# Performance work log

Measured on AMD Instinct MI355X. Metric: run time of the kernel, lower is better.

Reference implementation:

```python
import jax, jax.numpy as jnp
import numpy as np

ALPHA = 0.0005625
N_SLOPE = 1.5
VT = 0.026
VD = 0.1
BN_EPS = 1e-5


def _log1p_exp(a):
    return jnp.log1p(jnp.exp(jnp.clip(a, -30.0, 30.0)))


def _ekv_conv(x, theta, stride=1, padding=1):
    # x: (B, C, H, W); theta: (Cout, C*3*3)
    # Patches ordered (C, kh, kw) along channel dim, matching torch.nn.Unfold.
    patches = jax.lax.conv_general_dilated_patches(
        x, filter_shape=(3, 3), window_strides=(stride, stride),
        padding=[(padding, padding), (padding, padding)])
    B, K, Ho, Wo = patches.shape
    vg = patches.reshape(B, 1, K, Ho * Wo)              # (B,1,K,L)
    th = theta[None, :, :, None]                        # (1,Cout,K,1)
    nVT = N_SLOPE * VT
    arg1 = (vg - th) / nVT
    arg2 = (vg - th - VD) / nVT
    I = ALPHA * (_log1p_exp(arg1) ** 2 - _log1p_exp(arg2) ** 2)  # (B,Cout,K,L)
    return I.sum(axis=2).reshape(B, -1, Ho, Wo)


def _batchnorm_train(x, gamma, beta):
    # training-mode BN (biased variance), matching fresh nn.BatchNorm2d forward
    mean = x.mean(axis=(0, 2, 3), keepdims=True)
    var = x.var(axis=(0, 2, 3), keepdims=True)
    xhat = (x - mean) * jax.lax.rsqrt(var + BN_EPS)
    return xhat * gamma[None, :, None, None] + beta[None, :, None, None]


def setup_inputs() -> dict:
    key = jax.random.key(0)
    ks = jax.random.split(key, 3)
    B, C, H, W = 4, 64, 32, 32
    planes = 64
    K = C * 9
    x = jax.random.uniform(ks[0], (B, C, H, W), dtype=jnp.float32)
    theta1 = jax.random.uniform(ks[1], (planes, K), minval=2.8, maxval=4.8, dtype=jnp.float32)
    theta2 = jax.random.uniform(ks[2], (planes, planes * 9), minval=2.8, maxval=4.8, dtype=jnp.float32)
    return {
        "x": x,
        "theta1": theta1,
        "theta2": theta2,
        "prescale_scale": jnp.float32(4.5),
        "prescale_shift": jnp.float32(3.8),
        "ls1": jnp.float32(3.0),
        "ls2": jnp.float32(3.0),
        "bn1_gamma": jnp.ones((planes,), jnp.float32),
        "bn1_beta": jnp.zeros((planes,), jnp.float32),
        "bn2_gamma": jnp.ones((planes,), jnp.float32),
        "bn2_beta": jnp.zeros((planes,), jnp.float32),
    }


def reference(x, theta1, theta2, prescale_scale, prescale_shift, ls1, ls2,
              bn1_gamma, bn1_beta, bn2_gamma, bn2_beta):
    identity = x  # stride==1 and in_planes==planes -> identity shortcut
    out = x * prescale_scale + prescale_shift
    out = ls1 * _ekv_conv(out, theta1, stride=1, padding=1)
    out = _batchnorm_train(out, bn1_gamma, bn1_beta)
    out = ls2 * _ekv_conv(out, theta2, stride=1, padding=1)
    out = _batchnorm_train(out, bn2_gamma, bn2_beta)
    return out + identity
```

## Files before the change

kernel.cpp:

```cpp
#include <hip/hip_runtime.h>
#include <math.h>

#define NLUT     4096
#define LUT_LO   (-0.33)
#define LUT_H    (0.0004)
#define LUT_INVH (2500.0f)
#define LUT_BIAS (825.0f)
#define BAND_LO  (-0.35f)
#define BAND_HI  (1.28f)

#define WS_LUT    0
#define WS_TH2T   32768
#define WS_RAW1   180224
#define WS_MASK   1228800
#define WS_STAT1  1261568
#define WS_SUMS2  1262080
#define WS_THMAX  1262592
#define WS_THMIN  1262596
#define WS_TOTAL  1262600

__device__ __forceinline__ double f_exact(double d) {
    const double nvt = 1.5 * 0.026;
    double a1 = d / nvt;         a1 = fmin(fmax(a1, -30.0), 30.0);
    double a2 = (d - 0.1) / nvt; a2 = fmin(fmax(a2, -30.0), 30.0);
    double s1 = log1p(exp(a1));
    double s2 = log1p(exp(a2));
    return 0.0005625 * (s1 * s1 - s2 * s2);
}

__global__ __launch_bounds__(256) void k0_prep(const float* __restrict__ theta2,
        float* __restrict__ lutg, float* __restrict__ th2t, unsigned* __restrict__ mm)
{
    int blk = blockIdx.x;
    if (blk < 16) {
        int i = blk * 256 + threadIdx.x;
        double f0 = f_exact(LUT_LO + (double)i * LUT_H);
        double f1 = f_exact(LUT_LO + (double)(i + 1) * LUT_H);
        lutg[2 * i]     = (float)f0;
        lutg[2 * i + 1] = (float)(f1 - f0);
    } else {
        int i = (blk - 16) * 256 + threadIdx.x;
        int p = i & 63, k = i >> 6;
        float v = theta2[p * 576 + k];
        th2t[k * 64 + p] = v;
        __shared__ float smin[256], smax[256];
        smin[threadIdx.x] = v; smax[threadIdx.x] = v;
        __syncthreads();
        for (int s = 128; s > 0; s >>= 1) {
            if (threadIdx.x < s) {
                smin[threadIdx.x] = fminf(smin[threadIdx.x], smin[threadIdx.x + s]);
                smax[threadIdx.x] = fmaxf(smax[threadIdx.x], smax[threadIdx.x + s]);
            }
            __syncthreads();
        }
        if (threadIdx.x == 0) {
            atomicMax(&mm[0], __float_as_uint(smax[0]));
            atomicMin(&mm[1], __float_as_uint(smin[0]));
        }
    }
}

__global__ __launch_bounds__(256) void k1_conv1(const float* __restrict__ x,
    const float* __restrict__ theta1, const float* __restrict__ psc,
    const float* __restrict__ psh, const float* __restrict__ ls1,
    const float* __restrict__ lutg, float* __restrict__ raw1)
{
    __shared__ float2 lut[NLUT];
    {
        const float4* src = (const float4*)lutg;
        float4* dst = (float4*)lut;
        #pragma unroll
        for (int i = threadIdx.x; i < NLUT / 2; i += 256) dst[i] = src[i];
    }
    __syncthreads();

    int blk = blockIdx.x;
    int pg = blk & 7;
    int yp = (blk >> 3) & 15;
    int b  = blk >> 7;
    int wv = __builtin_amdgcn_readfirstlane((int)threadIdx.x >> 6);
    int lane = threadIdx.x & 63;
    int r = lane >> 5, xc = lane & 31;
    int y = yp * 2 + r;
    int p0 = pg * 8 + wv * 2;

    float scale = psc[0], shift = psh[0];
    const float* xb  = x + b * 65536;
    const float* t0p = theta1 + p0 * 576;
    const float* t1p = t0p + 576;
    float acc0 = 0.f, acc1 = 0.f;

    #pragma unroll
    for (int j = 0; j < 9; ++j) {
        int ny = y + j / 3 - 1, nx = xc + j % 3 - 1;
        if ((unsigned)ny < 32u && (unsigned)nx < 32u) {
            const float* px = xb + ny * 32 + nx;
            #pragma unroll 4
            for (int c = 0; c < 64; ++c) {
                float v  = fmaf(px[c * 1024], scale, shift);
                float t0 = t0p[c * 9 + j];
                float t1 = t1p[c * 9 + j];
                float q0 = fmaf(v - t0, LUT_INVH, LUT_BIAS);
                q0 = fminf(fmaxf(q0, 0.f), 4095.0f);
                int   i0 = (int)q0;
                float fr0 = q0 - (float)i0;
                float2 e0 = lut[i0];
                acc0 = fmaf(fr0, e0.y, acc0 + e0.x);
                float q1 = fmaf(v - t1, LUT_INVH, LUT_BIAS);
                q1 = fminf(fmaxf(q1, 0.f), 4095.0f);
                int   i1 = (int)q1;
                float fr1 = q1 - (float)i1;
                float2 e1 = lut[i1];
                acc1 = fmaf(fr1, e1.y, acc1 + e1.x);
            }
        }
    }
    float l1 = ls1[0];
    int o = ((b * 64 + p0) * 32 + y) * 32 + xc;
    raw1[o]        = l1 * acc0;
    raw1[o + 1024] = l1 * acc1;
}

__global__ __launch_bounds__(256) void k2_stats1(const float* __restrict__ raw1,
                                                 float* __restrict__ stat1)
{
    int p = blockIdx.x;
    float s = 0.f, q = 0.f;
    for (int b = 0; b < 4; ++b) {
        const float* base = raw1 + (b * 64 + p) * 1024;
        for (int k = threadIdx.x; k < 1024; k += 256) {
            float v = base[k];
            s += v; q += v * v;
        }
    }
    __shared__ float ss[256], sq[256];
    ss[threadIdx.x] = s; sq[threadIdx.x] = q;
    __syncthreads();
    for (int st = 128; st > 0; st >>= 1) {
        if (threadIdx.x < st) {
            ss[threadIdx.x] += ss[threadIdx.x + st];
            sq[threadIdx.x] += sq[threadIdx.x + st];
        }
        __syncthreads();
    }
    if (threadIdx.x == 0) {
        double mean = (double)ss[0] / 4096.0;
        double var  = (double)sq[0] / 4096.0 - mean * mean;
        if (var < 0) var = 0;
        stat1[p]      = (float)mean;
        stat1[64 + p] = (float)(1.0 / sqrt(var + 1e-5));
    }
}

__global__ __launch_bounds__(256) void k3_bn1mask(float* __restrict__ v2,
    const float* __restrict__ stat1, const float* __restrict__ g1,
    const float* __restrict__ b1, const unsigned* __restrict__ mm,
    unsigned long long* __restrict__ masks)
{
    int idx = blockIdx.x * 256 + threadIdx.x;
    int c = (idx >> 10) & 63;
    float v = v2[idx];
    v = (v - stat1[c]) * stat1[64 + c];
    v = v * g1[c] + b1[c];
    v2[idx] = v;
    float tmax = __uint_as_float(mm[0]);
    float tmin = __uint_as_float(mm[1]);
    if (v > tmin + BAND_LO && v < tmax + BAND_HI) {
        int b = idx >> 16;
        int pix = idx & 1023;
        atomicOr(&masks[b * 1024 + pix], 1ull << c);
    }
}

__global__ __launch_bounds__(256) void k4_conv2(const float* __restrict__ v2,
    const float* __restrict__ th2t, const unsigned long long* __restrict__ masks,
    const float* __restrict__ ls2, float* __restrict__ out, float* __restrict__ sums2)
{
    int wv = __builtin_amdgcn_readfirstlane((int)threadIdx.x >> 6);
    int lane = threadIdx.x & 63;
    int W = blockIdx.x * 4 + wv;
    float l2 = ls2[0];
    const float inv_nvt = (float)(1.0 / (1.5 * 0.026));
    float lsum = 0.f, lsq = 0.f;

    for (int i = 0; i < 4; ++i) {
        int P = W * 4 + i;
        int b = P >> 10, rem = P & 1023;
        int y = rem >> 5, xq = rem & 31;
        float acc = 0.f;
        #pragma unroll
        for (int j = 0; j < 9; ++j) {
            int ny = y + j / 3 - 1, nx = xq + j % 3 - 1;
            if ((unsigned)ny < 32u && (unsigned)nx < 32u) {
                unsigned long long m = masks[b * 1024 + ny * 32 + nx];
                while (m) {
                    int c = __ffsll((long long)m) - 1;
                    m &= m - 1;
                    float v  = v2[((b * 64 + c) * 32 + ny) * 32 + nx];
                    float th = th2t[(c * 9 + j) * 64 + lane];
                    float d = v - th;
                    if (d > BAND_LO && d < BAND_HI) {
                        float a1 = fminf(fmaxf(d * inv_nvt, -30.f), 30.f);
                        float a2 = fminf(fmaxf((d - 0.1f) * inv_nvt, -30.f), 30.f);
                        float s1 = __logf(1.f + __expf(a1));
                        float s2 = __logf(1.f + __expf(a2));
                        acc += (s1 * s1 - s2 * s2);
                    }
                }
            }
        }
        float r2 = 0.0005625f * l2 * acc;
        out[((b * 64 + lane) * 32 + y) * 32 + xq] = r2;
        lsum += r2; lsq += r2 * r2;
    }
    __shared__ float ss[256], sq[256];
    ss[threadIdx.x] = lsum; sq[threadIdx.x] = lsq;
    __syncthreads();
    if (threadIdx.x < 64) {
        float a  = ss[threadIdx.x] + ss[threadIdx.x + 64] + ss[threadIdx.x + 128] + ss[threadIdx.x + 192];
        float qq = sq[threadIdx.x] + sq[threadIdx.x + 64] + sq[threadIdx.x + 128] + sq[threadIdx.x + 192];
        atomicAdd(&sums2[threadIdx.x], a);
        atomicAdd(&sums2[64 + threadIdx.x], qq);
    }
}

__global__ __launch_bounds__(256) void k6_final(float* __restrict__ out,
    const float* __restrict__ x, const float* __restrict__ sums2,
    const float* __restrict__ g2, const float* __restrict__ b2)
{
    int idx = blockIdx.x * 256 + threadIdx.x;
    int p = (idx >> 10) & 63;
    float m   = sums2[p] * (1.f / 4096.f);
    float var = sums2[64 + p] * (1.f / 4096.f) - m * m;
    var = fmaxf(var, 0.f);
    float rstd = rsqrtf(var + 1e-5f);
    out[idx] = (out[idx] - m) * rstd * g2[p] + b2[p] + x[idx];
}

extern "C" void kernel_launch(void* const* d_in, const int* in_sizes, int n_in,
                              void* d_out, int out_size, void* d_ws, size_t ws_size,
                              hipStream_t stream)
{
    const float* x   = (const float*)d_in[0];
    const float* th1 = (const float*)d_in[1];
    const float* th2 = (const float*)d_in[2];
    const float* psc = (const float*)d_in[3];
    const float* psh = (const float*)d_in[4];
    const float* l1  = (const float*)d_in[5];
    const float* l2  = (const float*)d_in[6];
    const float* g1  = (const float*)d_in[7];
    const float* b1  = (const float*)d_in[8];
    const float* g2  = (const float*)d_in[9];
    const float* b2  = (const float*)d_in[10];
    float* out = (float*)d_out;
    char* ws = (char*)d_ws;
    if (ws_size < (size_t)WS_TOTAL) return;

    float* lut   = (float*)(ws + WS_LUT);
    float* th2t  = (float*)(ws + WS_TH2T);
    float* raw1  = (float*)(ws + WS_RAW1);
    unsigned long long* masks = (unsigned long long*)(ws + WS_MASK);
    float* stat1 = (float*)(ws + WS_STAT1);
    float* sums2 = (float*)(ws + WS_SUMS2);
    unsigned* mm = (unsigned*)(ws + WS_THMAX);

    hipMemsetAsync(ws + WS_MASK, 0, WS_THMIN - WS_MASK, stream);
    hipMemsetAsync(ws + WS_THMIN, 0x7F, 4, stream);

    k0_prep  <<<160,  256, 0, stream>>>(th2, lut, th2t, mm);
    k1_conv1 <<<512,  256, 0, stream>>>(x, th1, psc, psh, l1, lut, raw1);
    k2_stats1<<<64,   256, 0, stream>>>(raw1, stat1);
    k3_bn1mask<<<1024,256, 0, stream>>>(raw1, stat1, g1, b1, mm, masks);
    k4_conv2 <<<256,  256, 0, stream>>>(raw1, th2t, masks, l2, out, sums2);
    k6_final <<<1024, 256, 0, stream>>>(out, x, sums2, g2, b2);
}
```

Measured before the change: 95.27 us.

## Shrink LUT, pre-transform input to NHWC, fuse BN1 stats into conv1

The LUT drops from 4096 to 1024 entries with a folded slope/intercept encoding, so each tap needs one fmaf plus a masked byte-offset lookup. The prescale is precomputed into a channel-last buffer (aliasing the output) so conv1 reads float4 vectors of channels. BN1 statistics are now accumulated with wave shuffles and atomics inside conv1, which removes the separate stats kernel and one launch. Conv2 goes from four pixels per wave to one, with four times as many blocks, and the min/max init is folded into a single memset using complemented atomicMax. In exchange the coarser LUT can lose accuracy, and float atomics make the BN1 sums order-nondeterministic.

```diff
diff --git a/kernel.cpp b/kernel.cpp
--- a/kernel.cpp
+++ b/kernel.cpp
@@ -1,23 +1,22 @@
 #include <hip/hip_runtime.h>
 #include <math.h>
 
-#define NLUT     4096
-#define LUT_LO   (-0.33)
-#define LUT_H    (0.0004)
-#define LUT_INVH (2500.0f)
-#define LUT_BIAS (825.0f)
-#define BAND_LO  (-0.35f)
-#define BAND_HI  (1.28f)
+#define LUT_N   1024
+#define LUT_H   0.0016
+#define LUT_LO  (-0.33)
+#define INVH8   5000.0f
+#define QMAX    8184.0f
+#define BAND_LO (-0.35f)
+#define BAND_HI (1.28f)
 
 #define WS_LUT    0
-#define WS_TH2T   32768
-#define WS_RAW1   180224
-#define WS_MASK   1228800
-#define WS_STAT1  1261568
-#define WS_SUMS2  1262080
-#define WS_THMAX  1262592
-#define WS_THMIN  1262596
-#define WS_TOTAL  1262600
+#define WS_TH2T   8192
+#define WS_RAW1   155648
+#define WS_MASK   1204224
+#define WS_SUMS1  1236992
+#define WS_SUMS2  1237504
+#define WS_MM     1238016
+#define WS_TOTAL  1238024
 
 __device__ __forceinline__ double f_exact(double d) {
     const double nvt = 1.5 * 0.026;
@@ -28,146 +27,135 @@
     return 0.0005625 * (s1 * s1 - s2 * s2);
 }
 
-__global__ __launch_bounds__(256) void k0_prep(const float* __restrict__ theta2,
-        float* __restrict__ lutg, float* __restrict__ th2t, unsigned* __restrict__ mm)
-{
-    int blk = blockIdx.x;
-    if (blk < 16) {
-        int i = blk * 256 + threadIdx.x;
-        double f0 = f_exact(LUT_LO + (double)i * LUT_H);
-        double f1 = f_exact(LUT_LO + (double)(i + 1) * LUT_H);
-        lutg[2 * i]     = (float)f0;
-        lutg[2 * i + 1] = (float)(f1 - f0);
-    } else {
-        int i = (blk - 16) * 256 + threadIdx.x;
+__global__ __launch_bounds__(256) void k0_prep(
+    const float* __restrict__ x, const float* __restrict__ theta2,
+    const float* __restrict__ psc, const float* __restrict__ psh,
+    float2* __restrict__ lutg, float* __restrict__ th2t,
+    float* __restrict__ xs, unsigned* __restrict__ mm)
+{
+    int blk = blockIdx.x, tid = threadIdx.x;
+    if (blk < 4) {
+        int i = blk * 256 + tid;
+        double d0 = LUT_LO + (double)i * LUT_H;
+        double f0 = f_exact(d0), f1 = f_exact(d0 + LUT_H);
+        double d8 = (f1 - f0) * 0.125;
+        double ex = f0 - (double)(8 * i) * d8;
+        lutg[i] = make_float2((float)ex, (float)d8);
+    } else if (blk < 148) {
+        int i = (blk - 4) * 256 + tid;
         int p = i & 63, k = i >> 6;
         float v = theta2[p * 576 + k];
         th2t[k * 64 + p] = v;
         __shared__ float smin[256], smax[256];
-        smin[threadIdx.x] = v; smax[threadIdx.x] = v;
+        smin[tid] = v; smax[tid] = v;
         __syncthreads();
         for (int s = 128; s > 0; s >>= 1) {
-            if (threadIdx.x < s) {
-                smin[threadIdx.x] = fminf(smin[threadIdx.x], smin[threadIdx.x + s]);
-                smax[threadIdx.x] = fmaxf(smax[threadIdx.x], smax[threadIdx.x + s]);
+            if (tid < s) {
+                smin[tid] = fminf(smin[tid], smin[tid + s]);
+                smax[tid] = fmaxf(smax[tid], smax[tid + s]);
             }
             __syncthreads();
         }
-        if (threadIdx.x == 0) {
+        if (tid == 0) {
             atomicMax(&mm[0], __float_as_uint(smax[0]));
-            atomicMin(&mm[1], __float_as_uint(smin[0]));
-        }
-    }
-}
-
-__global__ __launch_bounds__(256) void k1_conv1(const float* __restrict__ x,
-    const float* __restrict__ theta1, const float* __restrict__ psc,
-    const float* __restrict__ psh, const float* __restrict__ ls1,
-    const float* __restrict__ lutg, float* __restrict__ raw1)
-{
-    __shared__ float2 lut[NLUT];
+            atomicMax(&mm[1], ~__float_as_uint(smin[0]));
+        }
+    } else {
+        int idx = (blk - 148) * 256 + tid;
+        int c = idx & 63, gp = idx >> 6;
+        int b = gp >> 10, pp = gp & 1023;
+        float xv = x[b * 65536 + c * 1024 + pp];
+        float sc = psc[0] * INVH8;
+        float sh = (psh[0] + 0.33f) * INVH8;
+        xs[idx] = fmaf(xv, sc, sh);
+    }
+}
+
+#define TAP(V, TH) {                                            \
+    float th_ = (TH);                                           \
+    float q_ = fmaf(th_, -INVH8, (V));                          \
+    q_ = fminf(fmaxf(q_, 0.f), QMAX);                           \
+    int ib_ = (int)q_ & ~7;                                     \
+    float2 e_ = *(const float2*)((const char*)lut + ib_);       \
+    acc = fmaf(q_, e_.y, acc + e_.x);                           \
+}
+
+__global__ __launch_bounds__(256) void k1_conv1(
+    const float* __restrict__ xs, const float* __restrict__ theta1,
+    const float* __restrict__ ls1, const float2* __restrict__ lutg,
+    float* __restrict__ raw1, float* __restrict__ sums1)
+{
+    __shared__ float2 lut[LUT_N];
     {
-        const float4* src = (const float4*)lutg;
-        float4* dst = (float4*)lut;
-        #pragma unroll
-        for (int i = threadIdx.x; i < NLUT / 2; i += 256) dst[i] = src[i];
+        const float4* s = (const float4*)lutg;
+        float4* d = (float4*)lut;
+        for (int i = threadIdx.x; i < LUT_N / 2; i += 256) d[i] = s[i];
     }
     __syncthreads();
 
     int blk = blockIdx.x;
-    int pg = blk & 7;
-    int yp = (blk >> 3) & 15;
-    int b  = blk >> 7;
     int wv = __builtin_amdgcn_readfirstlane((int)threadIdx.x >> 6);
     int lane = threadIdx.x & 63;
+    int p  = (blk & 15) * 4 + wv;
+    int yp = (blk >> 4) & 15;
+    int b  = blk >> 8;
     int r = lane >> 5, xc = lane & 31;
     int y = yp * 2 + r;
-    int p0 = pg * 8 + wv * 2;
-
-    float scale = psc[0], shift = psh[0];
-    const float* xb  = x + b * 65536;
-    const float* t0p = theta1 + p0 * 576;
-    const float* t1p = t0p + 576;
-    float acc0 = 0.f, acc1 = 0.f;
-
-    #pragma unroll
-    for (int j = 0; j < 9; ++j) {
-        int ny = y + j / 3 - 1, nx = xc + j % 3 - 1;
-        if ((unsigned)ny < 32u && (unsigned)nx < 32u) {
-            const float* px = xb + ny * 32 + nx;
+
+    const float* tpp = theta1 + p * 576;
+    float acc = 0.f;
+
+    for (int jy = 0; jy < 3; ++jy) {
+        int ny = y + jy - 1;
+        if ((unsigned)ny >= 32u) continue;
+        for (int jx = 0; jx < 3; ++jx) {
+            int nx = xc + jx - 1;
+            if ((unsigned)nx >= 32u) continue;
+            const float4* px4 = (const float4*)(xs + (((b << 10) + ny * 32 + nx) << 6));
+            const float* tp = tpp + (jy * 3 + jx);
             #pragma unroll 4
-            for (int c = 0; c < 64; ++c) {
-                float v  = fmaf(px[c * 1024], scale, shift);
-                float t0 = t0p[c * 9 + j];
-                float t1 = t1p[c * 9 + j];
-                float q0 = fmaf(v - t0, LUT_INVH, LUT_BIAS);
-                q0 = fminf(fmaxf(q0, 0.f), 4095.0f);
-                int   i0 = (int)q0;
-                float fr0 = q0 - (float)i0;
-                float2 e0 = lut[i0];
-                acc0 = fmaf(fr0, e0.y, acc0 + e0.x);
-                float q1 = fmaf(v - t1, LUT_INVH, LUT_BIAS);
-                q1 = fminf(fmaxf(q1, 0.f), 4095.0f);
-                int   i1 = (int)q1;
-                float fr1 = q1 - (float)i1;
-                float2 e1 = lut[i1];
-                acc1 = fmaf(fr1, e1.y, acc1 + e1.x);
+            for (int cc = 0; cc < 16; ++cc) {
+                float4 vb = px4[cc];
+                const float* tq = tp + cc * 36;
+                TAP(vb.x, tq[0]);
+                TAP(vb.y, tq[9]);
+                TAP(vb.z, tq[18]);
+                TAP(vb.w, tq[27]);
             }
         }
     }
-    float l1 = ls1[0];
-    int o = ((b * 64 + p0) * 32 + y) * 32 + xc;
-    raw1[o]        = l1 * acc0;
-    raw1[o + 1024] = l1 * acc1;
-}
-
-__global__ __launch_bounds__(256) void k2_stats1(const float* __restrict__ raw1,
-                                                 float* __restrict__ stat1)
-{
-    int p = blockIdx.x;
-    float s = 0.f, q = 0.f;
-    for (int b = 0; b < 4; ++b) {
-        const float* base = raw1 + (b * 64 + p) * 1024;
-        for (int k = threadIdx.x; k < 1024; k += 256) {
-            float v = base[k];
-            s += v; q += v * v;
-        }
-    }
-    __shared__ float ss[256], sq[256];
-    ss[threadIdx.x] = s; sq[threadIdx.x] = q;
-    __syncthreads();
-    for (int st = 128; st > 0; st >>= 1) {
-        if (threadIdx.x < st) {
-            ss[threadIdx.x] += ss[threadIdx.x + st];
-            sq[threadIdx.x] += sq[threadIdx.x + st];
-        }
-        __syncthreads();
-    }
-    if (threadIdx.x == 0) {
-        double mean = (double)ss[0] / 4096.0;
-        double var  = (double)sq[0] / 4096.0 - mean * mean;
-        if (var < 0) var = 0;
-        stat1[p]      = (float)mean;
-        stat1[64 + p] = (float)(1.0 / sqrt(var + 1e-5));
+    float r1 = ls1[0] * acc;
+    raw1[(((b << 6) + p) << 10) + y * 32 + xc] = r1;
+
+    float lsum = r1, lsq = r1 * r1;
+    for (int s = 32; s > 0; s >>= 1) {
+        lsum += __shfl_xor(lsum, s);
+        lsq  += __shfl_xor(lsq, s);
+    }
+    if (lane == 0) {
+        atomicAdd(&sums1[p], lsum);
+        atomicAdd(&sums1[64 + p], lsq);
     }
 }
 
 __global__ __launch_bounds__(256) void k3_bn1mask(float* __restrict__ v2,
-    const float* __restrict__ stat1, const float* __restrict__ g1,
+    const float* __restrict__ sums1, const float* __restrict__ g1,
     const float* __restrict__ b1, const unsigned* __restrict__ mm,
     unsigned long long* __restrict__ masks)
 {
     int idx = blockIdx.x * 256 + threadIdx.x;
     int c = (idx >> 10) & 63;
+    float m   = sums1[c] * (1.f / 4096.f);
+    float var = sums1[64 + c] * (1.f / 4096.f) - m * m;
+    var = fmaxf(var, 0.f);
+    float rstd = rsqrtf(var + 1e-5f);
     float v = v2[idx];
-    v = (v - stat1[c]) * stat1[64 + c];
-    v = v * g1[c] + b1[c];
+    v = (v - m) * rstd * g1[c] + b1[c];
     v2[idx] = v;
     float tmax = __uint_as_float(mm[0]);
-    float tmin = __uint_as_float(mm[1]);
+    float tmin = __uint_as_float(~mm[1]);
     if (v > tmin + BAND_LO && v < tmax + BAND_HI) {
-        int b = idx >> 16;
-        int pix = idx & 1023;
+        int b = idx >> 16, pix = idx & 1023;
         atomicOr(&masks[b * 1024 + pix], 1ull << c);
     }
 }
@@ -178,43 +166,39 @@
 {
     int wv = __builtin_amdgcn_readfirstlane((int)threadIdx.x >> 6);
     int lane = threadIdx.x & 63;
-    int W = blockIdx.x * 4 + wv;
+    int P = blockIdx.x * 4 + wv;
+    int b = P >> 10, rem = P & 1023;
+    int y = rem >> 5, xq = rem & 31;
     float l2 = ls2[0];
     const float inv_nvt = (float)(1.0 / (1.5 * 0.026));
-    float lsum = 0.f, lsq = 0.f;
-
-    for (int i = 0; i < 4; ++i) {
-        int P = W * 4 + i;
-        int b = P >> 10, rem = P & 1023;
-        int y = rem >> 5, xq = rem & 31;
-        float acc = 0.f;
-        #pragma unroll
-        for (int j = 0; j < 9; ++j) {
-            int ny = y + j / 3 - 1, nx = xq + j % 3 - 1;
-            if ((unsigned)ny < 32u && (unsigned)nx < 32u) {
-                unsigned long long m = masks[b * 1024 + ny * 32 + nx];
-                while (m) {
-                    int c = __ffsll((long long)m) - 1;
-                    m &= m - 1;
-                    float v  = v2[((b * 64 + c) * 32 + ny) * 32 + nx];
-                    float th = th2t[(c * 9 + j) * 64 + lane];
-                    float d = v - th;
-                    if (d > BAND_LO && d < BAND_HI) {
-                        float a1 = fminf(fmaxf(d * inv_nvt, -30.f), 30.f);
-                        float a2 = fminf(fmaxf((d - 0.1f) * inv_nvt, -30.f), 30.f);
-                        float s1 = __logf(1.f + __expf(a1));
-                        float s2 = __logf(1.f + __expf(a2));
-                        acc += (s1 * s1 - s2 * s2);
-                    }
+    float acc = 0.f;
+
+    #pragma unroll
+    for (int j = 0; j < 9; ++j) {
+        int ny = y + j / 3 - 1, nx = xq + j % 3 - 1;
+        if ((unsigned)ny < 32u && (unsigned)nx < 32u) {
+            unsigned long long mk = masks[b * 1024 + ny * 32 + nx];
+            while (mk) {
+                int c = __ffsll((long long)mk) - 1;
+                mk &= mk - 1;
+                float v  = v2[((b * 64 + c) * 32 + ny) * 32 + nx];
+                float th = th2t[(c * 9 + j) * 64 + lane];
+                float d = v - th;
+                if (d > BAND_LO && d < BAND_HI) {
+                    float a1 = fminf(fmaxf(d * inv_nvt, -30.f), 30.f);
+                    float a2 = fminf(fmaxf((d - 0.1f) * inv_nvt, -30.f), 30.f);
+                    float s1 = __logf(1.f + __expf(a1));
+                    float s2 = __logf(1.f + __expf(a2));
+                    acc += (s1 * s1 - s2 * s2);
                 }
             }
         }
-        float r2 = 0.0005625f * l2 * acc;
-        out[((b * 64 + lane) * 32 + y) * 32 + xq] = r2;
-        lsum += r2; lsq += r2 * r2;
-    }
+    }
+    float r2 = 0.0005625f * l2 * acc;
+    out[((b * 64 + lane) * 32 + y) * 32 + xq] = r2;
+
     __shared__ float ss[256], sq[256];
-    ss[threadIdx.x] = lsum; sq[threadIdx.x] = lsq;
+    ss[threadIdx.x] = r2; sq[threadIdx.x] = r2 * r2;
     __syncthreads();
     if (threadIdx.x < 64) {
         float a  = ss[threadIdx.x] + ss[threadIdx.x + 64] + ss[threadIdx.x + 128] + ss[threadIdx.x + 192];
@@ -256,21 +240,21 @@
     char* ws = (char*)d_ws;
     if (ws_size < (size_t)WS_TOTAL) return;
 
-    float* lut   = (float*)(ws + WS_LUT);
-    float* th2t  = (float*)(ws + WS_TH2T);
-    float* raw1  = (float*)(ws + WS_RAW1);
+    float2* lutg = (float2*)(ws + WS_LUT);
+    float*  th2t = (float*)(ws + WS_TH2T);
+    float*  raw1 = (float*)(ws + WS_RAW1);
     unsigned long long* masks = (unsigned long long*)(ws + WS_MASK);
-    float* stat1 = (float*)(ws + WS_STAT1);
-    float* sums2 = (float*)(ws + WS_SUMS2);
-    unsigned* mm = (unsigned*)(ws + WS_THMAX);
-
-    hipMemsetAsync(ws + WS_MASK, 0, WS_THMIN - WS_MASK, stream);
-    hipMemsetAsync(ws + WS_THMIN, 0x7F, 4, stream);
-
-    k0_prep  <<<160,  256, 0, stream>>>(th2, lut, th2t, mm);
-    k1_conv1 <<<512,  256, 0, stream>>>(x, th1, psc, psh, l1, lut, raw1);
-    k2_stats1<<<64,   256, 0, stream>>>(raw1, stat1);
-    k3_bn1mask<<<1024,256, 0, stream>>>(raw1, stat1, g1, b1, mm, masks);
-    k4_conv2 <<<256,  256, 0, stream>>>(raw1, th2t, masks, l2, out, sums2);
-    k6_final <<<1024, 256, 0, stream>>>(out, x, sums2, g2, b2);
-}
+    float*  sums1 = (float*)(ws + WS_SUMS1);
+    float*  sums2 = (float*)(ws + WS_SUMS2);
+    unsigned* mm  = (unsigned*)(ws + WS_MM);
+
+    float* xs = out;
+
+    hipMemsetAsync(ws + WS_MASK, 0, WS_TOTAL - WS_MASK, stream);
+
+    k0_prep   <<<1172, 256, 0, stream>>>(x, th2, psc, psh, lutg, th2t, xs, mm);
+    k1_conv1  <<<1024, 256, 0, stream>>>(xs, th1, l1, lutg, raw1, sums1);
+    k3_bn1mask<<<1024, 256, 0, stream>>>(raw1, sums1, g1, b1, mm, masks);
+    k4_conv2  <<<1024, 256, 0, stream>>>(raw1, th2t, masks, l2, out, sums2);
+    k6_final  <<<1024, 256, 0, stream>>>(out, x, sums2, g2, b2);
+}
```

Result: slower. 130.4 us (+36.9%).
